# Kernel optimization log

Measured on AMD Instinct MI355X. Metric: run time of the kernel, lower is better.

## Reference

```python
import jax, jax.numpy as jnp
import numpy as np

FEAT = 256
L = 8          # max_evi_length (chain length)
MC = 8         # max_chain
N = 4096       # examples
B = N * MC


def setup_inputs() -> dict:
    key = jax.random.key(0)
    ks = jax.random.split(key, 8)
    x = jax.random.normal(ks[0], (B, L, FEAT), dtype=jnp.float32)
    # end_inds: one-hot float indicator of chain end position (>=1)
    pos = jax.random.randint(ks[1], (B,), 1, L)
    end_inds = jax.nn.one_hot(pos, L, dtype=jnp.float32)
    s_in = 1.0 / np.sqrt(2 * FEAT)
    s_d = 1.0 / np.sqrt(FEAT)
    Wc = jax.random.uniform(ks[2], (FEAT, 2 * FEAT), minval=-s_in, maxval=s_in, dtype=jnp.float32)
    bc = jax.random.uniform(ks[3], (FEAT,), minval=-s_in, maxval=s_in, dtype=jnp.float32)
    Wcs = jax.random.uniform(ks[4], (FEAT, FEAT), minval=-s_d, maxval=s_d, dtype=jnp.float32)
    Wanti = jax.random.uniform(ks[5], (FEAT, 2 * FEAT), minval=-s_in, maxval=s_in, dtype=jnp.float32)
    Wout = jax.random.uniform(ks[6], (2, 2 * FEAT), minval=-s_in, maxval=s_in, dtype=jnp.float32)
    bout = jax.random.uniform(ks[7], (2,), minval=-s_in, maxval=s_in, dtype=jnp.float32)
    return dict(x=x, end_inds=end_inds, max_chain=MC, Wc=Wc, bc=bc,
                Wcs=Wcs, Wanti=Wanti, Wout=Wout, bout=bout)


def _forward(x, end_inds, max_chain, Wc, bc, Wcs, Wanti, Wout, bout):
    Bx, Lx, d = x.shape
    h_c0 = jnp.swapaxes(x[:, :-1, :], 0, 1)   # [L-1, B, d]
    h_e0 = jnp.swapaxes(x[:, 1:, :], 0, 1)    # [L-1, B, d]
    # anti_updater(cat([h_c0, h_e0])) precomputed (depends only on x)
    anti = jnp.concatenate([h_c0, h_e0], -1) @ Wanti.T  # [L-1, B, d]
    s0 = x[:, 0, :]                           # initial s_anti

    def step(s, inp):
        hc0, he0, a = inp
        # note: original uses state_updater_c for BOTH h_c and h_e
        h_c = jnp.concatenate([s, hc0], -1) @ Wc.T + bc
        h_e = jnp.concatenate([s, he0], -1) @ Wc.T + bc
        cs = jax.nn.sigmoid(jnp.sum((h_c @ Wcs.T) * h_e, -1))  # [B]
        s_new = jnp.tanh(cs[:, None] * a) + s
        return s_new, (cs, s_new)

    _, (cs_ls, s_ls) = jax.lax.scan(step, s0, (h_c0, h_e0, anti))
    cs_ls = cs_ls.T                    # [B, L-1]
    s_ls = jnp.swapaxes(s_ls, 0, 1)    # [B, L-1, d]

    cum_cs = jnp.cumprod(cs_ls, axis=-1)
    ei = end_inds[:, 1:]               # [B, L-1]
    cum = (cum_cs * ei).sum(-1) - (1.0 - ei.sum(-1)) * 10000.0
    cum = jax.nn.softmax(cum.reshape(-1, max_chain), axis=-1)   # [N, MC]

    s_sel = (s_ls * ei[:, :, None]).sum(1)           # [B, d]
    s_sel = s_sel.reshape(-1, max_chain, d)          # [N, MC, d]
    u = jnp.einsum('nmd,nm->nd', s_sel, cum)         # bmm over chains
    u = jnp.concatenate([x[::max_chain, 0], u], -1)  # [N, 2d]
    return u @ Wout.T + bout                         # [N, 2]


def reference(x, end_inds, max_chain, Wc, bc, Wcs, Wanti, Wout, bout):
    return _forward(x, end_inds, max_chain, Wc, bc, Wcs, Wanti, Wout, bout)
```

## Files before the change

### kernel.cpp

```cpp
#include <hip/hip_runtime.h>
#include <hip/hip_bf16.h>

#define FEATN 256
#define XROW  2048
#define MT    64
#define NW    16
#define LDST  264
#define TILE  (MT * LDST)
#define NSTEP 7

using f32x4 = __attribute__((ext_vector_type(4))) float;
using s16x8 = __attribute__((ext_vector_type(8))) short;

__device__ __forceinline__ short f2bf(float f) {
  __hip_bfloat16 h = __float2bfloat16(f);
  return *reinterpret_cast<short*>(&h);
}

__device__ __forceinline__ f32x4 ntload4(const float* p) {
  return __builtin_nontemporal_load(reinterpret_cast<const f32x4*>(p));
}

__device__ __forceinline__ s16x8 pack8(const f32x4 a, const f32x4 b) {
  s16x8 r;
  r[0] = f2bf(a[0]); r[1] = f2bf(a[1]); r[2] = f2bf(a[2]); r[3] = f2bf(a[3]);
  r[4] = f2bf(b[0]); r[5] = f2bf(b[1]); r[6] = f2bf(b[2]); r[7] = f2bf(b[3]);
  return r;
}

__device__ __forceinline__ float dpp_red16(float x) {
  x += __int_as_float(__builtin_amdgcn_update_dpp(0, __float_as_int(x), 0xB1, 0xF, 0xF, true));
  x += __int_as_float(__builtin_amdgcn_update_dpp(0, __float_as_int(x), 0x4E, 0xF, 0xF, true));
  x += __int_as_float(__builtin_amdgcn_update_dpp(0, __float_as_int(x), 0x141, 0xF, 0xF, true));
  x += __int_as_float(__builtin_amdgcn_update_dpp(0, __float_as_int(x), 0x140, 0xF, 0xF, true));
  return x;
}

__global__ void prep_kernel(const float* __restrict__ Wc, const float* __restrict__ bc,
                            const float* __restrict__ Wcs, const float* __restrict__ Wanti,
                            short* __restrict__ Wt, float* __restrict__ bq) {
  __shared__ float wrow[FEATN];
  __shared__ float red[FEATN];
  const int n = blockIdx.x, k = threadIdx.x;
  wrow[k] = Wcs[n * FEATN + k];
  __syncthreads();
  float a0 = 0.f, a1 = 0.f;
  #pragma unroll 8
  for (int j = 0; j < FEATN; ++j) {
    const float w = wrow[j];
    a0 += w * Wc[j * 512 + k];
    a1 += w * Wc[j * 512 + 256 + k];
  }
  red[k] = wrow[k] * bc[k];
  __syncthreads();
  for (int off = 128; off > 0; off >>= 1) {
    if (k < off) red[k] += red[k + off];
    __syncthreads();
  }
  if (k == 0) bq[n] = red[0];
  const int fo = (n >> 4) * 4096 + (k >> 5) * 512 + (((k >> 3) & 3) * 16 + (n & 15)) * 8 + (k & 7);
  Wt[0 * 65536 + fo] = f2bf(a0);
  Wt[1 * 65536 + fo] = f2bf(a1);
  Wt[2 * 65536 + fo] = f2bf(Wc[n * 512 + k]);
  Wt[3 * 65536 + fo] = f2bf(Wc[n * 512 + 256 + k]);
  Wt[4 * 65536 + fo] = f2bf(Wanti[n * 512 + k]);
  Wt[5 * 65536 + fo] = f2bf(Wanti[n * 512 + 256 + k]);
}

__global__ __launch_bounds__(1024, 4)
void chain_kernel(const float* __restrict__ x, const float* __restrict__ endi,
                  const short* __restrict__ Wt, const float* __restrict__ bq,
                  const float* __restrict__ bc, const float* __restrict__ Wout,
                  const float* __restrict__ bout, float* __restrict__ out) {
  __shared__ short sbuf[2 * TILE];
  __shared__ float redP[MT][NW];
  __shared__ float selP[MT][2 * NW];
  __shared__ float cpL[MT], cumL[MT], seL[MT], csL[MT], eiL[MT];

  const int tid  = (int)threadIdx.x;
  const int lane = tid & 63;
  const int wave = tid >> 6;
  const int lr   = lane & 15;
  const int lh   = lane >> 4;
  const int r0   = (int)blockIdx.x * MT;

  if (tid < MT) { cpL[tid] = 1.f; cumL[tid] = 0.f; seL[tid] = 0.f; }
  #pragma unroll
  for (int i = 0; i < 2; ++i) (&selP[0][0])[i * 1024 + tid] = 0.f;

  #pragma unroll
  for (int i = 0; i < 2; ++i) {
    const int f = i * 8192 + tid * 8;
    const int row = f >> 8, col = f & 255;
    const float* src = &x[(size_t)(r0 + row) * XROW + col];
    const s16x8 b = pack8(ntload4(src), ntload4(src + 4));
    *reinterpret_cast<s16x8*>(&sbuf[row * LDST + col]) = b;
    *reinterpret_cast<s16x8*>(&sbuf[TILE + row * LDST + col]) = b;
  }

  const int wcol = wave * 16 + lr;
  const short* wfb = Wt + wave * 4096 + lane * 8;
  const int abase = lr * LDST + lh * 8;
  const float bqv = bq[wcol];
  const float bcv = bc[wcol];
  const float wo0 = Wout[256 + wcol];
  const float wo1 = Wout[768 + wcol];
  const f32x4 fzero = {0.f, 0.f, 0.f, 0.f};

  float sreg[4][4];
  #pragma unroll
  for (int m = 0; m < 4; ++m)
    #pragma unroll
    for (int e = 0; e < 4; ++e)
      sreg[m][e] = x[(size_t)(r0 + m * 16 + lh * 4 + e) * XROW + wcol];

  __syncthreads();

  for (int t = 0; t < NSTEP; ++t) {
    const int so = (t & 1) * TILE;
    const int xo = ((t + 1) & 1) * TILE;

    f32x4 AccA[4], AccB[4], AccN[4];
    #pragma unroll
    for (int m = 0; m < 4; ++m) { AccA[m] = fzero; AccB[m] = fzero; AccN[m] = fzero; }

    #pragma unroll 1
    for (int ks = 0; ks < 8; ++ks) {
      const short* p = wfb + ks * 512;
      {
        const s16x8 b0 = *reinterpret_cast<const s16x8*>(p + 0 * 65536);
        const s16x8 b2 = *reinterpret_cast<const s16x8*>(p + 2 * 65536);
        #pragma unroll
        for (int m = 0; m < 4; ++m) {
          const s16x8 a_s = *reinterpret_cast<const s16x8*>(&sbuf[so + abase + m * (16 * LDST) + ks * 32]);
          AccA[m] = __builtin_amdgcn_mfma_f32_16x16x32_bf16(a_s, b0, AccA[m], 0, 0, 0);
          AccB[m] = __builtin_amdgcn_mfma_f32_16x16x32_bf16(a_s, b2, AccB[m], 0, 0, 0);
        }
      }
      {
        const s16x8 b1 = *reinterpret_cast<const s16x8*>(p + 1 * 65536);
        const s16x8 b4 = *reinterpret_cast<const s16x8*>(p + 4 * 65536);
        #pragma unroll
        for (int m = 0; m < 4; ++m) {
          const s16x8 a_x = *reinterpret_cast<const s16x8*>(&sbuf[xo + abase + m * (16 * LDST) + ks * 32]);
          AccA[m] = __builtin_amdgcn_mfma_f32_16x16x32_bf16(a_x, b1, AccA[m], 0, 0, 0);
          AccN[m] = __builtin_amdgcn_mfma_f32_16x16x32_bf16(a_x, b4, AccN[m], 0, 0, 0);
        }
      }
    }
    __syncthreads();

    #pragma unroll
    for (int i = 0; i < 2; ++i) {
      const int f = i * 8192 + tid * 8;
      const int row = f >> 8, col = f & 255;
      const float* src = &x[(size_t)(r0 + row) * XROW + (t + 1) * FEATN + col];
      const s16x8 b = pack8(ntload4(src), ntload4(src + 4));
      *reinterpret_cast<s16x8*>(&sbuf[so + row * LDST + col]) = b;
    }
    __syncthreads();

    #pragma unroll 1
    for (int ks = 0; ks < 8; ++ks) {
      const short* p = wfb + ks * 512;
      const s16x8 b3 = *reinterpret_cast<const s16x8*>(p + 3 * 65536);
      const s16x8 b5 = *reinterpret_cast<const s16x8*>(p + 5 * 65536);
      #pragma unroll
      for (int m = 0; m < 4; ++m) {
        const s16x8 a_n = *reinterpret_cast<const s16x8*>(&sbuf[so + abase + m * (16 * LDST) + ks * 32]);
        AccB[m] = __builtin_amdgcn_mfma_f32_16x16x32_bf16(a_n, b3, AccB[m], 0, 0, 0);
        AccN[m] = __builtin_amdgcn_mfma_f32_16x16x32_bf16(a_n, b5, AccN[m], 0, 0, 0);
      }
    }

    #pragma unroll
    for (int m = 0; m < 4; ++m) {
      #pragma unroll
      for (int e = 0; e < 4; ++e) {
        const float p = dpp_red16((AccA[m][e] + bqv) * (AccB[m][e] + bcv));
        if (lr == 0) redP[m * 16 + lh * 4 + e][wave] = p;
      }
    }
    __syncthreads();

    if (tid < MT) {
      float d = 0.f;
      #pragma unroll
      for (int w = 0; w < NW; ++w) d += redP[tid][w];
      const float cs = 1.f / (1.f + __expf(-d));
      const float cp = cpL[tid] * cs;
      cpL[tid] = cp;
      const float ei = endi[(size_t)(r0 + tid) * 8 + (t + 1)];
      cumL[tid] += cp * ei;
      seL[tid] += ei;
      csL[tid] = cs;
      eiL[tid] = ei;
    }
    __syncthreads();

    #pragma unroll
    for (int m = 0; m < 4; ++m) {
      #pragma unroll
      for (int e = 0; e < 4; ++e) {
        const int row = m * 16 + lh * 4 + e;
        const float cs = csL[row];
        const float ag = cs * AccN[m][e];
        const float ex = __expf(2.f * ag);
        const float th = 1.f - 2.f / (ex + 1.f);
        const float sn = sreg[m][e] + th;
        sreg[m][e] = sn;
        sbuf[xo + row * LDST + wcol] = f2bf(sn);
        if (eiL[row] != 0.f) {
          const float p0 = dpp_red16(sn * wo0);
          const float p1 = dpp_red16(sn * wo1);
          if (lr == 0) { selP[row][wave * 2] = p0; selP[row][wave * 2 + 1] = p1; }
        }
      }
    }
    __syncthreads();
  }

  if (wave < 8) {
    const int g = wave;
    const int rowb = g * 8;
    float c[8];
    float mx = -3.4e38f;
    #pragma unroll
    for (int m = 0; m < 8; ++m) {
      c[m] = cumL[rowb + m] - (1.f - seL[rowb + m]) * 10000.f;
      mx = fmaxf(mx, c[m]);
    }
    float sum = 0.f;
    float wgt[8];
    #pragma unroll
    for (int m = 0; m < 8; ++m) { wgt[m] = __expf(c[m] - mx); sum += wgt[m]; }
    const float inv = 1.f / sum;
    float up0 = 0.f, up1 = 0.f;
    #pragma unroll
    for (int m = 0; m < 8; ++m) {
      float s0 = 0.f, s1 = 0.f;
      #pragma unroll
      for (int w = 0; w < NW; ++w) {
        s0 += selP[rowb + m][w * 2];
        s1 += selP[rowb + m][w * 2 + 1];
      }
      const float wm = wgt[m] * inv;
      up0 += wm * s0; up1 += wm * s1;
    }
    const int d = lane * 4;
    const float4 xv  = *reinterpret_cast<const float4*>(&x[(size_t)(r0 + rowb) * XROW + d]);
    const float4 w00 = *reinterpret_cast<const float4*>(&Wout[d]);
    const float4 w10 = *reinterpret_cast<const float4*>(&Wout[512 + d]);
    float o0 = xv.x * w00.x + xv.y * w00.y + xv.z * w00.z + xv.w * w00.w;
    float o1 = xv.x * w10.x + xv.y * w10.y + xv.z * w10.z + xv.w * w10.w;
    #pragma unroll
    for (int off = 1; off < 64; off <<= 1) {
      o0 += __shfl_xor(o0, off);
      o1 += __shfl_xor(o1, off);
    }
    if (lane == 0) {
      const int n = (int)blockIdx.x * 8 + g;
      out[n * 2 + 0] = o0 + up0 + bout[0];
      out[n * 2 + 1] = o1 + up1 + bout[1];
    }
  }
}

extern "C" void kernel_launch(void* const* d_in, const int* in_sizes, int n_in,
                              void* d_out, int out_size, void* d_ws, size_t ws_size,
                              hipStream_t stream) {
  const float* x     = (const float*)d_in[0];
  const float* endi  = (const float*)d_in[1];
  const float* Wc    = (const float*)d_in[3];
  const float* bc    = (const float*)d_in[4];
  const float* Wcs   = (const float*)d_in[5];
  const float* Wanti = (const float*)d_in[6];
  const float* Wout  = (const float*)d_in[7];
  const float* bout  = (const float*)d_in[8];
  float* out = (float*)d_out;

  char* ws = (char*)d_ws;
  short* Wt = (short*)ws;
  float* bq = (float*)(ws + 786432);

  prep_kernel<<<dim3(256), dim3(256), 0, stream>>>(Wc, bc, Wcs, Wanti, Wt, bq);
  chain_kernel<<<dim3(512), dim3(1024), 0, stream>>>(x, endi, Wt, bq, bc, Wout, bout, out);
}
```

Measured before the change: 257.4 us.

## Retile per-wave MFMA work into 32x32 blocks across row and column groups

```diff
diff --git a/kernel.cpp b/kernel.cpp
--- a/kernel.cpp
+++ b/kernel.cpp
@@ -4,7 +4,6 @@
 #define FEATN 256
 #define XROW  2048
 #define MT    64
-#define NW    16
 #define LDST  264
 #define TILE  (MT * LDST)
 #define NSTEP 7
@@ -73,8 +72,8 @@
                   const float* __restrict__ bc, const float* __restrict__ Wout,
                   const float* __restrict__ bout, float* __restrict__ out) {
   __shared__ short sbuf[2 * TILE];
-  __shared__ float redP[MT][NW];
-  __shared__ float selP[MT][2 * NW];
+  __shared__ float redP[MT][9];
+  __shared__ float selP[MT][17];
   __shared__ float cpL[MT], cumL[MT], seL[MT], csL[MT], eiL[MT];
 
   const int tid  = (int)threadIdx.x;
@@ -82,11 +81,12 @@
   const int wave = tid >> 6;
   const int lr   = lane & 15;
   const int lh   = lane >> 4;
+  const int rg   = wave >> 3;
+  const int cg   = wave & 7;
   const int r0   = (int)blockIdx.x * MT;
 
   if (tid < MT) { cpL[tid] = 1.f; cumL[tid] = 0.f; seL[tid] = 0.f; }
-  #pragma unroll
-  for (int i = 0; i < 2; ++i) (&selP[0][0])[i * 1024 + tid] = 0.f;
+  for (int i = tid; i < MT * 17; i += 1024) (&selP[0][0])[i] = 0.f;
 
   #pragma unroll
   for (int i = 0; i < 2; ++i) {
@@ -98,21 +98,23 @@
     *reinterpret_cast<s16x8*>(&sbuf[TILE + row * LDST + col]) = b;
   }
 
-  const int wcol = wave * 16 + lr;
-  const short* wfb = Wt + wave * 4096 + lane * 8;
-  const int abase = lr * LDST + lh * 8;
-  const float bqv = bq[wcol];
-  const float bcv = bc[wcol];
-  const float wo0 = Wout[256 + wcol];
-  const float wo1 = Wout[768 + wcol];
+  const int wc0 = cg * 32 + lr;
+  const short* wfb = Wt + cg * 8192 + lane * 8;
+  const int abase = (rg * 32 + lr) * LDST + lh * 8;
+  const float bqv0 = bq[wc0], bqv1 = bq[wc0 + 16];
+  const float bcv0 = bc[wc0], bcv1 = bc[wc0 + 16];
+  const float wo00 = Wout[256 + wc0], wo01 = Wout[256 + wc0 + 16];
+  const float wo10 = Wout[768 + wc0], wo11 = Wout[768 + wc0 + 16];
   const f32x4 fzero = {0.f, 0.f, 0.f, 0.f};
 
-  float sreg[4][4];
+  float sreg[2][2][4];
   #pragma unroll
-  for (int m = 0; m < 4; ++m)
-    #pragma unroll
-    for (int e = 0; e < 4; ++e)
-      sreg[m][e] = x[(size_t)(r0 + m * 16 + lh * 4 + e) * XROW + wcol];
+  for (int m = 0; m < 2; ++m)
+    #pragma unroll
+    for (int nn = 0; nn < 2; ++nn)
+      #pragma unroll
+      for (int e = 0; e < 4; ++e)
+        sreg[m][nn][e] = x[(size_t)(r0 + rg * 32 + m * 16 + lh * 4 + e) * XROW + cg * 32 + nn * 16 + lr];
 
   __syncthreads();
 
@@ -120,31 +122,47 @@
     const int so = (t & 1) * TILE;
     const int xo = ((t + 1) & 1) * TILE;
 
-    f32x4 AccA[4], AccB[4], AccN[4];
-    #pragma unroll
-    for (int m = 0; m < 4; ++m) { AccA[m] = fzero; AccB[m] = fzero; AccN[m] = fzero; }
+    f32x4 AccA[2][2], AccB[2][2], AccN[2][2];
+    #pragma unroll
+    for (int m = 0; m < 2; ++m)
+      #pragma unroll
+      for (int nn = 0; nn < 2; ++nn) { AccA[m][nn] = fzero; AccB[m][nn] = fzero; AccN[m][nn] = fzero; }
 
     #pragma unroll 1
     for (int ks = 0; ks < 8; ++ks) {
       const short* p = wfb + ks * 512;
       {
-        const s16x8 b0 = *reinterpret_cast<const s16x8*>(p + 0 * 65536);
-        const s16x8 b2 = *reinterpret_cast<const s16x8*>(p + 2 * 65536);
-        #pragma unroll
-        for (int m = 0; m < 4; ++m) {
+        s16x8 b0[2], b2[2];
+        #pragma unroll
+        for (int nn = 0; nn < 2; ++nn) {
+          b0[nn] = *reinterpret_cast<const s16x8*>(p + nn * 4096 + 0 * 65536);
+          b2[nn] = *reinterpret_cast<const s16x8*>(p + nn * 4096 + 2 * 65536);
+        }
+        #pragma unroll
+        for (int m = 0; m < 2; ++m) {
           const s16x8 a_s = *reinterpret_cast<const s16x8*>(&sbuf[so + abase + m * (16 * LDST) + ks * 32]);
-          AccA[m] = __builtin_amdgcn_mfma_f32_16x16x32_bf16(a_s, b0, AccA[m], 0, 0, 0);
-          AccB[m] = __builtin_amdgcn_mfma_f32_16x16x32_bf16(a_s, b2, AccB[m], 0, 0, 0);
+          #pragma unroll
+          for (int nn = 0; nn < 2; ++nn) {
+            AccA[m][nn] = __builtin_amdgcn_mfma_f32_16x16x32_bf16(a_s, b0[nn], AccA[m][nn], 0, 0, 0);
+            AccB[m][nn] = __builtin_amdgcn_mfma_f32_16x16x32_bf16(a_s, b2[nn], AccB[m][nn], 0, 0, 0);
+          }
         }
       }
       {
-        const s16x8 b1 = *reinterpret_cast<const s16x8*>(p + 1 * 65536);
-        const s16x8 b4 = *reinterpret_cast<const s16x8*>(p + 4 * 65536);
-        #pragma unroll
-        for (int m = 0; m < 4; ++m) {
+        s16x8 b1[2], b4[2];
+        #pragma unroll
+        for (int nn = 0; nn < 2; ++nn) {
+          b1[nn] = *reinterpret_cast<const s16x8*>(p + nn * 4096 + 1 * 65536);
+          b4[nn] = *reinterpret_cast<const s16x8*>(p + nn * 4096 + 4 * 65536);
+        }
+        #pragma unroll
+        for (int m = 0; m < 2; ++m) {
           const s16x8 a_x = *reinterpret_cast<const s16x8*>(&sbuf[xo + abase + m * (16 * LDST) + ks * 32]);
-          AccA[m] = __builtin_amdgcn_mfma_f32_16x16x32_bf16(a_x, b1, AccA[m], 0, 0, 0);
-          AccN[m] = __builtin_amdgcn_mfma_f32_16x16x32_bf16(a_x, b4, AccN[m], 0, 0, 0);
+          #pragma unroll
+          for (int nn = 0; nn < 2; ++nn) {
+            AccA[m][nn] = __builtin_amdgcn_mfma_f32_16x16x32_bf16(a_x, b1[nn], AccA[m][nn], 0, 0, 0);
+            AccN[m][nn] = __builtin_amdgcn_mfma_f32_16x16x32_bf16(a_x, b4[nn], AccN[m][nn], 0, 0, 0);
+          }
         }
       }
     }
@@ -163,22 +181,31 @@
     #pragma unroll 1
     for (int ks = 0; ks < 8; ++ks) {
       const short* p = wfb + ks * 512;
-      const s16x8 b3 = *reinterpret_cast<const s16x8*>(p + 3 * 65536);
-      const s16x8 b5 = *reinterpret_cast<const s16x8*>(p + 5 * 65536);
-      #pragma unroll
-      for (int m = 0; m < 4; ++m) {
+      s16x8 b3[2], b5[2];
+      #pragma unroll
+      for (int nn = 0; nn < 2; ++nn) {
+        b3[nn] = *reinterpret_cast<const s16x8*>(p + nn * 4096 + 3 * 65536);
+        b5[nn] = *reinterpret_cast<const s16x8*>(p + nn * 4096 + 5 * 65536);
+      }
+      #pragma unroll
+      for (int m = 0; m < 2; ++m) {
         const s16x8 a_n = *reinterpret_cast<const s16x8*>(&sbuf[so + abase + m * (16 * LDST) + ks * 32]);
-        AccB[m] = __builtin_amdgcn_mfma_f32_16x16x32_bf16(a_n, b3, AccB[m], 0, 0, 0);
-        AccN[m] = __builtin_amdgcn_mfma_f32_16x16x32_bf16(a_n, b5, AccN[m], 0, 0, 0);
-      }
-    }
-
-    #pragma unroll
-    for (int m = 0; m < 4; ++m) {
+        #pragma unroll
+        for (int nn = 0; nn < 2; ++nn) {
+          AccB[m][nn] = __builtin_amdgcn_mfma_f32_16x16x32_bf16(a_n, b3[nn], AccB[m][nn], 0, 0, 0);
+          AccN[m][nn] = __builtin_amdgcn_mfma_f32_16x16x32_bf16(a_n, b5[nn], AccN[m][nn], 0, 0, 0);
+        }
+      }
+    }
+
+    #pragma unroll
+    for (int m = 0; m < 2; ++m) {
       #pragma unroll
       for (int e = 0; e < 4; ++e) {
-        const float p = dpp_red16((AccA[m][e] + bqv) * (AccB[m][e] + bcv));
-        if (lr == 0) redP[m * 16 + lh * 4 + e][wave] = p;
+        float p = (AccA[m][0][e] + bqv0) * (AccB[m][0][e] + bcv0)
+                + (AccA[m][1][e] + bqv1) * (AccB[m][1][e] + bcv1);
+        p = dpp_red16(p);
+        if (lr == 0) redP[rg * 32 + m * 16 + lh * 4 + e][cg] = p;
       }
     }
     __syncthreads();
@@ -186,7 +213,7 @@
     if (tid < MT) {
       float d = 0.f;
       #pragma unroll
-      for (int w = 0; w < NW; ++w) d += redP[tid][w];
+      for (int w = 0; w < 8; ++w) d += redP[tid][w];
       const float cs = 1.f / (1.f + __expf(-d));
       const float cp = cpL[tid] * cs;
       cpL[tid] = cp;
@@ -199,21 +226,26 @@
     __syncthreads();
 
     #pragma unroll
-    for (int m = 0; m < 4; ++m) {
+    for (int m = 0; m < 2; ++m) {
       #pragma unroll
       for (int e = 0; e < 4; ++e) {
-        const int row = m * 16 + lh * 4 + e;
+        const int row = rg * 32 + m * 16 + lh * 4 + e;
         const float cs = csL[row];
-        const float ag = cs * AccN[m][e];
-        const float ex = __expf(2.f * ag);
-        const float th = 1.f - 2.f / (ex + 1.f);
-        const float sn = sreg[m][e] + th;
-        sreg[m][e] = sn;
-        sbuf[xo + row * LDST + wcol] = f2bf(sn);
+        float sn2[2];
+        #pragma unroll
+        for (int nn = 0; nn < 2; ++nn) {
+          const float ag = cs * AccN[m][nn][e];
+          const float ex = __expf(2.f * ag);
+          const float th = 1.f - 2.f / (ex + 1.f);
+          const float sn = sreg[m][nn][e] + th;
+          sreg[m][nn][e] = sn;
+          sn2[nn] = sn;
+          sbuf[xo + row * LDST + (cg * 32 + nn * 16 + lr)] = f2bf(sn);
+        }
         if (eiL[row] != 0.f) {
-          const float p0 = dpp_red16(sn * wo0);
-          const float p1 = dpp_red16(sn * wo1);
-          if (lr == 0) { selP[row][wave * 2] = p0; selP[row][wave * 2 + 1] = p1; }
+          const float p0 = dpp_red16(sn2[0] * wo00 + sn2[1] * wo01);
+          const float p1 = dpp_red16(sn2[0] * wo10 + sn2[1] * wo11);
+          if (lr == 0) { selP[row][cg * 2] = p0; selP[row][cg * 2 + 1] = p1; }
         }
       }
     }
@@ -240,7 +272,7 @@
     for (int m = 0; m < 8; ++m) {
       float s0 = 0.f, s1 = 0.f;
       #pragma unroll
-      for (int w = 0; w < NW; ++w) {
+      for (int w = 0; w < 8; ++w) {
         s0 += selP[rowb + m][w * 2];
         s1 += selP[rowb + m][w * 2 + 1];
       }
```

After: 289.6 us. 1.13x slower.
